# Performance work log

Measured on AMD Instinct MI355X. Metric: run time of the kernel, lower is better.

Reference implementation:

```python
import jax, jax.numpy as jnp
import numpy as np

PAD = 0  # module-level global in the original repo (MT convention)


def setup_inputs() -> dict:
    key = jax.random.key(0)
    k1, k2, k3 = jax.random.split(key, 3)
    N, V, D = 2048, 32000, 512
    # realistic log-probabilities over the vocab
    pred_ll = jax.nn.log_softmax(jax.random.normal(k1, (N, V), jnp.float32), axis=-1)
    target = jax.random.randint(k2, (N,), 0, V)
    # frozen pretrained word-vector table (nn.Embedding.from_pretrained)
    emb = jax.random.normal(k3, (V, D), jnp.float32)
    return {"pred_ll": pred_ll, "target": target, "emb": emb}


def reference(pred_ll, target, emb):
    # pred_ll: [N, V] log-probs; target: [N] int ids; emb: [V, D] frozen table
    mask = (target != PAD).astype(pred_ll.dtype)  # [N] non-pad mask

    # nll_loss = -pred_ll.gather(-1, target) summed over non-pad tokens
    nll = -jnp.take_along_axis(pred_ll, target[:, None], axis=-1)[:, 0]  # [N]
    nll_loss = jnp.sum(nll * mask)

    # pairwise L2 distance gold-embedding vs full table, via the GEMM identity
    # ||g - e||^2 = ||g||^2 + ||e||^2 - 2 g.e  (avoids the [N, V, D] tensor)
    g = emb[target]                                    # [N, D]
    g2 = jnp.sum(g * g, axis=-1, keepdims=True)        # [N, 1]
    e2 = jnp.sum(emb * emb, axis=-1)[None, :]          # [1, V]
    d2 = jnp.maximum(g2 + e2 - 2.0 * (g @ emb.T), 0.0)  # [N, V]
    dist = jnp.sqrt(jnp.maximum(d2, 1e-12))             # [N, V], L2 distances

    dist_max = jnp.max(dist, axis=1, keepdims=True)    # [N, 1]
    w = jax.nn.softmax(dist_max - jnp.abs(dist), axis=1)  # [N, V]

    # loss = sum_v softmax_weight * (-log p), summed over non-pad tokens
    loss = jnp.sum(w * (-pred_ll), axis=1)             # [N]
    return (jnp.sum(loss * mask), nll_loss)
```

## Files before the change

### kernel.cpp

```cpp
#include <hip/hip_runtime.h>
#include <hip/hip_bf16.h>
#include <float.h>

#define NTOK   2048
#define VOCAB  32000
#define DIM    512
#define NCHUNK 128
#define NTILES 2000
#define ROWSB  256
#define NRB    (NTOK / ROWSB)
#define TILE_BYTES 16384

typedef __attribute__((ext_vector_type(4))) float  f32x4;
typedef __attribute__((ext_vector_type(8))) short  bf16x8;
typedef unsigned int u32;

__device__ __forceinline__ short f2bf(float f) {
    unsigned u = __builtin_bit_cast(unsigned, f);
    u = (u + 0x7FFFu + ((u >> 16) & 1u)) >> 16;
    return (short)u;
}

__device__ __forceinline__ void async_copy16(void* lds, const void* g) {
    __builtin_amdgcn_global_load_lds(
        (const __attribute__((address_space(1))) u32*)(const u32*)g,
        (__attribute__((address_space(3))) u32*)(u32*)lds, 16, 0, 0);
}

__global__ void init_out(float* out) {
    if (threadIdx.x < 2) out[threadIdx.x] = 0.f;
}

__global__ __launch_bounds__(256) void precast_kernel(
    const float* __restrict__ emb, short* __restrict__ Bbf, float* __restrict__ e2) {
    const int tile = blockIdx.x;
    const int t = threadIdx.x, w = t >> 6, l = t & 63;
    const int v0 = tile * 16;
    char* tbase = (char*)Bbf + (size_t)tile * TILE_BYTES;
    #pragma unroll
    for (int it = 0; it < 4; ++it) {
        const int v = it * 4 + w;
        const int j = l;
        const float* src = emb + (size_t)(v0 + v) * DIM + j * 8;
        f32x4 x0 = *(const f32x4*)src;
        f32x4 x1 = *(const f32x4*)(src + 4);
        bf16x8 b;
        b[0]=f2bf(x0.x); b[1]=f2bf(x0.y); b[2]=f2bf(x0.z); b[3]=f2bf(x0.w);
        b[4]=f2bf(x1.x); b[5]=f2bf(x1.y); b[6]=f2bf(x1.z); b[7]=f2bf(x1.w);
        float sq = x0.x*x0.x + x0.y*x0.y + x0.z*x0.z + x0.w*x0.w
                 + x1.x*x1.x + x1.y*x1.y + x1.z*x1.z + x1.w*x1.w;
        #pragma unroll
        for (int m = 1; m < 64; m <<= 1) sq += __shfl_xor(sq, m);
        if (l == 0) e2[v0 + v] = sq;
        const int addr = v * 1024 + ((j * 16) ^ ((v & 7) << 4));
        *(bf16x8*)(tbase + addr) = b;
    }
}

__global__ __launch_bounds__(256) void e2_kernel(const float* __restrict__ emb,
                                                 float* __restrict__ e2) {
    int gid = blockIdx.x * 256 + threadIdx.x;
    int wid = gid >> 6, l = gid & 63;
    if (wid >= VOCAB) return;
    const float* row = emb + (size_t)wid * DIM + l * 8;
    f32x4 a = *(const f32x4*)row;
    f32x4 b = *(const f32x4*)(row + 4);
    float s = a.x*a.x + a.y*a.y + a.z*a.z + a.w*a.w
            + b.x*b.x + b.y*b.y + b.z*b.z + b.w*b.w;
    #pragma unroll
    for (int m = 1; m < 64; m <<= 1) s += __shfl_xor(s, m);
    if (l == 0) e2[wid] = s;
}

template<bool PRECAST>
__global__ __launch_bounds__(512, 2) void fused_kernel(
    const float* __restrict__ pred_ll, const int* __restrict__ target,
    const float* __restrict__ emb, const short* __restrict__ Bbf,
    const float* __restrict__ e2g,
    float* __restrict__ partials ) {

    const int rb = blockIdx.x;
    const int ch = blockIdx.y;
    const int t  = threadIdx.x;
    const int w  = t >> 6;
    const int l  = t & 63;
    const int l15 = l & 15;
    const int lg  = l >> 4;

    __shared__ short ldsb[2][16 * DIM];

    const int t0 = (ch * NTILES) >> 7;
    const int t1 = ((ch + 1) * NTILES) >> 7;
    const int rowbase = rb * ROWSB + w * 32;

    bf16x8 afrag[2][16];
    #pragma unroll
    for (int s = 0; s < 2; ++s) {
        const int grow = target[rowbase + s * 16 + l15];
        if constexpr (PRECAST) {
            const char* abase = (const char*)Bbf + (size_t)(grow >> 4) * TILE_BYTES
                              + (grow & 15) * 1024;
            const int aswz = (grow & 7) << 4;
            #pragma unroll
            for (int ks = 0; ks < 16; ++ks)
                afrag[s][ks] = *(const bf16x8*)(abase + (((ks * 4 + lg) * 16) ^ aswz));
        } else {
            const float* gsrc = emb + (size_t)grow * DIM;
            #pragma unroll
            for (int ks = 0; ks < 16; ++ks) {
                const int k0 = ks * 32 + lg * 8;
                f32x4 x0 = *(const f32x4*)(gsrc + k0);
                f32x4 x1 = *(const f32x4*)(gsrc + k0 + 4);
                bf16x8 a;
                a[0]=f2bf(x0.x); a[1]=f2bf(x0.y); a[2]=f2bf(x0.z); a[3]=f2bf(x0.w);
                a[4]=f2bf(x1.x); a[5]=f2bf(x1.y); a[6]=f2bf(x1.z); a[7]=f2bf(x1.w);
                afrag[s][ks] = a;
            }
        }
    }
    float g2[2][4];
    #pragma unroll
    for (int s = 0; s < 2; ++s)
        #pragma unroll
        for (int r = 0; r < 4; ++r)
            g2[s][r] = e2g[target[rowbase + s * 16 + lg * 4 + r]];

    float s_[2][4] = {{0,0,0,0},{0,0,0,0}};
    float ac_[2][4] = {{0,0,0,0},{0,0,0,0}};

    auto stage = [&](int buf, int tg) {
        if constexpr (PRECAST) {
            const char* src = (const char*)Bbf + (size_t)tg * TILE_BYTES;
            char* dst = (char*)&ldsb[buf][0];
            async_copy16(dst + t * 16, src + t * 16);
            async_copy16(dst + 8192 + t * 16, src + 8192 + t * 16);
        } else {
            const int v0 = tg * 16;
            #pragma unroll
            for (int it = 0; it < 2; ++it) {
                const int c = it * 512 + t;
                const int v = c >> 6, j = c & 63;
                const float* src = emb + (size_t)(v0 + v) * DIM + j * 8;
                f32x4 x0 = *(const f32x4*)src;
                f32x4 x1 = *(const f32x4*)(src + 4);
                bf16x8 b;
                b[0]=f2bf(x0.x); b[1]=f2bf(x0.y); b[2]=f2bf(x0.z); b[3]=f2bf(x0.w);
                b[4]=f2bf(x1.x); b[5]=f2bf(x1.y); b[6]=f2bf(x1.z); b[7]=f2bf(x1.w);
                const int addr = v * 1024 + ((j * 16) ^ ((v & 7) << 4));
                *(bf16x8*)((char*)&ldsb[buf][0] + addr) = b;
            }
        }
    };

    stage(0, t0);
    __syncthreads();

    int cur = 0;
    const int swz = (l15 & 7) << 4;
    for (int tg = t0; tg < t1; ++tg) {
        if (tg + 1 < t1) stage(cur ^ 1, tg + 1);

        const int v0 = tg * 16;
        const float e2v = e2g[v0 + l15];
        float q[2][4];
        {
            const size_t p0 = (size_t)rowbase * VOCAB + v0 + l15;
            #pragma unroll
            for (int s = 0; s < 2; ++s)
                #pragma unroll
                for (int r = 0; r < 4; ++r)
                    q[s][r] = pred_ll[p0 + (size_t)(s * 16 + lg * 4 + r) * VOCAB];
        }

        f32x4 accs[2] = {{0,0,0,0},{0,0,0,0}};
        const char* lb = (const char*)&ldsb[cur][0];
        #pragma unroll
        for (int ks = 0; ks < 16; ++ks) {
            const int inner = (ks * 64 + lg * 16) ^ swz;
            bf16x8 b = *(const bf16x8*)(lb + l15 * 1024 + inner);
            accs[0] = __builtin_amdgcn_mfma_f32_16x16x32_bf16(afrag[0][ks], b, accs[0], 0, 0, 0);
            accs[1] = __builtin_amdgcn_mfma_f32_16x16x32_bf16(afrag[1][ks], b, accs[1], 0, 0, 0);
        }

        #pragma unroll
        for (int s = 0; s < 2; ++s)
            #pragma unroll
            for (int r = 0; r < 4; ++r) {
                float d2 = fmaxf(fmaf(-2.f, accs[s][r], g2[s][r] + e2v), 1e-12f);
                const float e = __expf(-sqrtf(d2));
                s_[s][r] += e;
                ac_[s][r] = fmaf(e, -q[s][r], ac_[s][r]);
            }

        __syncthreads();
        cur ^= 1;
    }

    #pragma unroll
    for (int s = 0; s < 2; ++s)
        #pragma unroll
        for (int r = 0; r < 4; ++r) {
            float sv = s_[s][r], av = ac_[s][r];
            #pragma unroll
            for (int m = 1; m < 16; m <<= 1) {
                sv += __shfl_xor(sv, m);
                av += __shfl_xor(av, m);
            }
            if (l15 == 0) {
                const int rg = rowbase + s * 16 + lg * 4 + r;
                float* pp = partials + ((size_t)rg * NCHUNK + ch) * 2;
                pp[0] = sv; pp[1] = av;
            }
        }
}

__global__ __launch_bounds__(256) void reduce_kernel(
    const float* __restrict__ pred_ll, const int* __restrict__ target,
    const float* __restrict__ partials, float* __restrict__ out) {
    const int row = blockIdx.x * 256 + threadIdx.x;
    float loss = 0.f, nll = 0.f;
    if (row < NTOK) {
        const int tg = target[row];
        const float mask = (tg != 0) ? 1.f : 0.f;
        const float* pp = partials + (size_t)row * NCHUNK * 2;
        float S = 0.f, A = 0.f;
        #pragma unroll 8
        for (int c = 0; c < NCHUNK; ++c) { S += pp[c * 2]; A += pp[c * 2 + 1]; }
        loss = mask * (A / S);
        nll  = mask * (-pred_ll[(size_t)row * VOCAB + tg]);
    }
    #pragma unroll
    for (int o = 32; o > 0; o >>= 1) {
        loss += __shfl_xor(loss, o);
        nll  += __shfl_xor(nll, o);
    }
    if ((threadIdx.x & 63) == 0) {
        atomicAdd(&out[0], loss);
        atomicAdd(&out[1], nll);
    }
}

extern "C" void kernel_launch(void* const* d_in, const int* in_sizes, int n_in,
                              void* d_out, int out_size, void* d_ws, size_t ws_size,
                              hipStream_t stream) {
    const float* pred_ll = (const float*)d_in[0];
    const int*   target  = (const int*)d_in[1];
    const float* emb     = (const float*)d_in[2];
    float* out = (float*)d_out;

    float* e2       = (float*)d_ws;
    float* partials = e2 + VOCAB;
    const size_t base = (size_t)VOCAB * 4 + (size_t)NTOK * NCHUNK * 2 * 4;
    short* Bbf      = (short*)((char*)d_ws + base);
    const size_t need = base + (size_t)NTILES * TILE_BYTES;
    const bool precast = (ws_size >= need);

    hipLaunchKernelGGL(init_out, dim3(1), dim3(64), 0, stream, out);
    if (precast) {
        hipLaunchKernelGGL(precast_kernel, dim3(NTILES), dim3(256), 0, stream, emb, Bbf, e2);
        hipLaunchKernelGGL((fused_kernel<true>), dim3(NRB, NCHUNK), dim3(512), 0, stream,
                           pred_ll, target, emb, Bbf, e2, partials);
    } else {
        hipLaunchKernelGGL(e2_kernel, dim3(VOCAB * 64 / 256), dim3(256), 0, stream, emb, e2);
        hipLaunchKernelGGL((fused_kernel<false>), dim3(NRB, NCHUNK), dim3(512), 0, stream,
                           pred_ll, target, emb, Bbf, e2, partials);
    }
    hipLaunchKernelGGL(reduce_kernel, dim3(NTOK / 256), dim3(256), 0, stream,
                       pred_ll, target, partials, out);
}
```

Baseline: 180.4 us.

## Stage pred_ll tiles into LDS asynchronously and halve block rows

```diff
diff --git a/kernel.cpp b/kernel.cpp
--- a/kernel.cpp
+++ b/kernel.cpp
@@ -7,9 +7,10 @@
 #define DIM    512
 #define NCHUNK 128
 #define NTILES 2000
-#define ROWSB  256
+#define ROWSB  128
 #define NRB    (NTOK / ROWSB)
 #define TILE_BYTES 16384
+#define QTILE_BYTES 8192
 
 typedef __attribute__((ext_vector_type(4))) float  f32x4;
 typedef __attribute__((ext_vector_type(8))) short  bf16x8;
@@ -25,6 +26,10 @@
     __builtin_amdgcn_global_load_lds(
         (const __attribute__((address_space(1))) u32*)(const u32*)g,
         (__attribute__((address_space(3))) u32*)(u32*)lds, 16, 0, 0);
+}
+
+__device__ __forceinline__ int qswz(int addr) {
+    return addr ^ (((addr >> 8) & 1) << 6);
 }
 
 __global__ void init_out(float* out) {
@@ -73,7 +78,7 @@
 }
 
 template<bool PRECAST>
-__global__ __launch_bounds__(512, 2) void fused_kernel(
+__global__ __launch_bounds__(256, 2) void fused_kernel(
     const float* __restrict__ pred_ll, const int* __restrict__ target,
     const float* __restrict__ emb, const short* __restrict__ Bbf,
     const float* __restrict__ e2g,
@@ -87,11 +92,13 @@
     const int l15 = l & 15;
     const int lg  = l >> 4;
 
-    __shared__ short ldsb[2][16 * DIM];
+    __shared__ char ldsB[2][TILE_BYTES];
+    __shared__ char ldsQ[2][QTILE_BYTES];
 
     const int t0 = (ch * NTILES) >> 7;
     const int t1 = ((ch + 1) * NTILES) >> 7;
-    const int rowbase = rb * ROWSB + w * 32;
+    const int rowblk = rb * ROWSB;
+    const int rowbase = rowblk + w * 32;
 
     bf16x8 afrag[2][16];
     #pragma unroll
@@ -129,51 +136,66 @@
     float ac_[2][4] = {{0,0,0,0},{0,0,0,0}};
 
     auto stage = [&](int buf, int tg) {
+        const int v0 = tg * 16;
         if constexpr (PRECAST) {
-            const char* src = (const char*)Bbf + (size_t)tg * TILE_BYTES;
-            char* dst = (char*)&ldsb[buf][0];
-            async_copy16(dst + t * 16, src + t * 16);
-            async_copy16(dst + 8192 + t * 16, src + 8192 + t * 16);
+            const char* srcB = (const char*)Bbf + (size_t)tg * TILE_BYTES;
+            char* dstB = ldsB[buf];
+            #pragma unroll
+            for (int it = 0; it < 4; ++it)
+                async_copy16(dstB + it * 4096 + t * 16, srcB + it * 4096 + t * 16);
         } else {
-            const int v0 = tg * 16;
             #pragma unroll
             for (int it = 0; it < 2; ++it) {
-                const int c = it * 512 + t;
-                const int v = c >> 6, j = c & 63;
-                const float* src = emb + (size_t)(v0 + v) * DIM + j * 8;
+                const int c = it * 256 + t;
+                const int v = c >> 5, j = c & 31;
+                const float* src = emb + (size_t)(v0 + v) * DIM + j * 16;
                 f32x4 x0 = *(const f32x4*)src;
                 f32x4 x1 = *(const f32x4*)(src + 4);
-                bf16x8 b;
-                b[0]=f2bf(x0.x); b[1]=f2bf(x0.y); b[2]=f2bf(x0.z); b[3]=f2bf(x0.w);
-                b[4]=f2bf(x1.x); b[5]=f2bf(x1.y); b[6]=f2bf(x1.z); b[7]=f2bf(x1.w);
-                const int addr = v * 1024 + ((j * 16) ^ ((v & 7) << 4));
-                *(bf16x8*)((char*)&ldsb[buf][0] + addr) = b;
-            }
+                f32x4 x2 = *(const f32x4*)(src + 8);
+                f32x4 x3 = *(const f32x4*)(src + 12);
+                bf16x8 b0, b1;
+                b0[0]=f2bf(x0.x); b0[1]=f2bf(x0.y); b0[2]=f2bf(x0.z); b0[3]=f2bf(x0.w);
+                b0[4]=f2bf(x1.x); b0[5]=f2bf(x1.y); b0[6]=f2bf(x1.z); b0[7]=f2bf(x1.w);
+                b1[0]=f2bf(x2.x); b1[1]=f2bf(x2.y); b1[2]=f2bf(x2.z); b1[3]=f2bf(x2.w);
+                b1[4]=f2bf(x3.x); b1[5]=f2bf(x3.y); b1[6]=f2bf(x3.z); b1[7]=f2bf(x3.w);
+                const int a0 = v * 1024 + (((j * 2    ) * 16) ^ ((v & 7) << 4));
+                const int a1 = v * 1024 + (((j * 2 + 1) * 16) ^ ((v & 7) << 4));
+                *(bf16x8*)(ldsB[buf] + a0) = b0;
+                *(bf16x8*)(ldsB[buf] + a1) = b1;
+            }
+        }
+        char* dstQ = ldsQ[buf];
+        #pragma unroll
+        for (int it = 0; it < 2; ++it) {
+            const int p = (it * 256 + t) * 16;
+            const int a = qswz(p);
+            const int row = a >> 6, c16 = (a >> 4) & 3;
+            const float* src = pred_ll + (size_t)(rowblk + row) * VOCAB + v0 + c16 * 4;
+            async_copy16(dstQ + p, src);
         }
     };
 
     stage(0, t0);
-    __syncthreads();
 
     int cur = 0;
     const int swz = (l15 & 7) << 4;
     for (int tg = t0; tg < t1; ++tg) {
-        if (tg + 1 < t1) stage(cur ^ 1, tg + 1);
+        if (tg + 1 < t1) {
+            stage(cur ^ 1, tg + 1);
+            if constexpr (PRECAST)
+                asm volatile("s_waitcnt vmcnt(6)" ::: "memory");
+            else
+                asm volatile("s_waitcnt vmcnt(2) lgkmcnt(0)" ::: "memory");
+        } else {
+            asm volatile("s_waitcnt vmcnt(0) lgkmcnt(0)" ::: "memory");
+        }
+        __builtin_amdgcn_s_barrier();
 
         const int v0 = tg * 16;
         const float e2v = e2g[v0 + l15];
-        float q[2][4];
-        {
-            const size_t p0 = (size_t)rowbase * VOCAB + v0 + l15;
-            #pragma unroll
-            for (int s = 0; s < 2; ++s)
-                #pragma unroll
-                for (int r = 0; r < 4; ++r)
-                    q[s][r] = pred_ll[p0 + (size_t)(s * 16 + lg * 4 + r) * VOCAB];
-        }
 
         f32x4 accs[2] = {{0,0,0,0},{0,0,0,0}};
-        const char* lb = (const char*)&ldsb[cur][0];
+        const char* lb = ldsB[cur];
         #pragma unroll
         for (int ks = 0; ks < 16; ++ks) {
             const int inner = (ks * 64 + lg * 16) ^ swz;
@@ -182,17 +204,21 @@
             accs[1] = __builtin_amdgcn_mfma_f32_16x16x32_bf16(afrag[1][ks], b, accs[1], 0, 0, 0);
         }
 
+        const char* lq = ldsQ[cur];
         #pragma unroll
         for (int s = 0; s < 2; ++s)
             #pragma unroll
             for (int r = 0; r < 4; ++r) {
+                const int rloc = w * 32 + s * 16 + lg * 4 + r;
+                const float q = *(const float*)(lq + qswz(rloc * 64 + l15 * 4));
                 float d2 = fmaxf(fmaf(-2.f, accs[s][r], g2[s][r] + e2v), 1e-12f);
                 const float e = __expf(-sqrtf(d2));
                 s_[s][r] += e;
-                ac_[s][r] = fmaf(e, -q[s][r], ac_[s][r]);
-            }
-
-        __syncthreads();
+                ac_[s][r] = fmaf(e, -q, ac_[s][r]);
+            }
+
+        asm volatile("" ::: "memory");
+        __builtin_amdgcn_s_barrier();
         cur ^= 1;
     }
 
@@ -258,11 +284,11 @@
     hipLaunchKernelGGL(init_out, dim3(1), dim3(64), 0, stream, out);
     if (precast) {
         hipLaunchKernelGGL(precast_kernel, dim3(NTILES), dim3(256), 0, stream, emb, Bbf, e2);
-        hipLaunchKernelGGL((fused_kernel<true>), dim3(NRB, NCHUNK), dim3(512), 0, stream,
+        hipLaunchKernelGGL((fused_kernel<true>), dim3(NRB, NCHUNK), dim3(256), 0, stream,
                            pred_ll, target, emb, Bbf, e2, partials);
     } else {
         hipLaunchKernelGGL(e2_kernel, dim3(VOCAB * 64 / 256), dim3(256), 0, stream, emb, e2);
-        hipLaunchKernelGGL((fused_kernel<false>), dim3(NRB, NCHUNK), dim3(512), 0, stream,
+        hipLaunchKernelGGL((fused_kernel<false>), dim3(NRB, NCHUNK), dim3(256), 0, stream,
                            pred_ll, target, emb, Bbf, e2, partials);
     }
     hipLaunchKernelGGL(reduce_kernel, dim3(NTOK / 256), dim3(256), 0, stream,
```

New measurement: 179.6 us. Within noise of the previous version (-0.4%).

## Load B fragments directly to registers, dropping LDS staging and block sync

Applied to the files above, without the earlier changes.

```diff
diff --git a/kernel.cpp b/kernel.cpp
--- a/kernel.cpp
+++ b/kernel.cpp
@@ -7,13 +7,12 @@
 #define DIM    512
 #define NCHUNK 128
 #define NTILES 2000
-#define ROWSB  256
+#define ROWSB  128
 #define NRB    (NTOK / ROWSB)
 #define TILE_BYTES 16384
 
 typedef __attribute__((ext_vector_type(4))) float  f32x4;
 typedef __attribute__((ext_vector_type(8))) short  bf16x8;
-typedef unsigned int u32;
 
 __device__ __forceinline__ short f2bf(float f) {
     unsigned u = __builtin_bit_cast(unsigned, f);
@@ -21,10 +20,11 @@
     return (short)u;
 }
 
-__device__ __forceinline__ void async_copy16(void* lds, const void* g) {
-    __builtin_amdgcn_global_load_lds(
-        (const __attribute__((address_space(1))) u32*)(const u32*)g,
-        (__attribute__((address_space(3))) u32*)(u32*)lds, 16, 0, 0);
+__device__ __forceinline__ bf16x8 cvt8(f32x4 a, f32x4 b) {
+    bf16x8 r;
+    r[0]=f2bf(a.x); r[1]=f2bf(a.y); r[2]=f2bf(a.z); r[3]=f2bf(a.w);
+    r[4]=f2bf(b.x); r[5]=f2bf(b.y); r[6]=f2bf(b.z); r[7]=f2bf(b.w);
+    return r;
 }
 
 __global__ void init_out(float* out) {
@@ -40,20 +40,16 @@
     #pragma unroll
     for (int it = 0; it < 4; ++it) {
         const int v = it * 4 + w;
-        const int j = l;
-        const float* src = emb + (size_t)(v0 + v) * DIM + j * 8;
+        const float* src = emb + (size_t)(v0 + v) * DIM + l * 8;
         f32x4 x0 = *(const f32x4*)src;
         f32x4 x1 = *(const f32x4*)(src + 4);
-        bf16x8 b;
-        b[0]=f2bf(x0.x); b[1]=f2bf(x0.y); b[2]=f2bf(x0.z); b[3]=f2bf(x0.w);
-        b[4]=f2bf(x1.x); b[5]=f2bf(x1.y); b[6]=f2bf(x1.z); b[7]=f2bf(x1.w);
         float sq = x0.x*x0.x + x0.y*x0.y + x0.z*x0.z + x0.w*x0.w
                  + x1.x*x1.x + x1.y*x1.y + x1.z*x1.z + x1.w*x1.w;
         #pragma unroll
         for (int m = 1; m < 64; m <<= 1) sq += __shfl_xor(sq, m);
         if (l == 0) e2[v0 + v] = sq;
-        const int addr = v * 1024 + ((j * 16) ^ ((v & 7) << 4));
-        *(bf16x8*)(tbase + addr) = b;
+        char* dst = tbase + (l >> 2) * 1024 + (((l & 3) * 16 + v) * 16);
+        *(bf16x8*)dst = cvt8(x0, x1);
     }
 }
 
@@ -73,7 +69,7 @@
 }
 
 template<bool PRECAST>
-__global__ __launch_bounds__(512, 2) void fused_kernel(
+__global__ __launch_bounds__(256, 2) void fused_kernel(
     const float* __restrict__ pred_ll, const int* __restrict__ target,
     const float* __restrict__ emb, const short* __restrict__ Bbf,
     const float* __restrict__ e2g,
@@ -82,12 +78,10 @@
     const int rb = blockIdx.x;
     const int ch = blockIdx.y;
     const int t  = threadIdx.x;
-    const int w  = t >> 6;
     const int l  = t & 63;
     const int l15 = l & 15;
     const int lg  = l >> 4;
-
-    __shared__ short ldsb[2][16 * DIM];
+    const int w   = t >> 6;
 
     const int t0 = (ch * NTILES) >> 7;
     const int t1 = ((ch + 1) * NTILES) >> 7;
@@ -98,23 +92,18 @@
     for (int s = 0; s < 2; ++s) {
         const int grow = target[rowbase + s * 16 + l15];
         if constexpr (PRECAST) {
-            const char* abase = (const char*)Bbf + (size_t)(grow >> 4) * TILE_BYTES
-                              + (grow & 15) * 1024;
-            const int aswz = (grow & 7) << 4;
+            const char* ab = (const char*)Bbf + (size_t)(grow >> 4) * TILE_BYTES
+                           + ((l & 48) + (grow & 15)) * 16;
             #pragma unroll
             for (int ks = 0; ks < 16; ++ks)
-                afrag[s][ks] = *(const bf16x8*)(abase + (((ks * 4 + lg) * 16) ^ aswz));
+                afrag[s][ks] = *(const bf16x8*)(ab + ks * 1024);
         } else {
             const float* gsrc = emb + (size_t)grow * DIM;
             #pragma unroll
             for (int ks = 0; ks < 16; ++ks) {
                 const int k0 = ks * 32 + lg * 8;
-                f32x4 x0 = *(const f32x4*)(gsrc + k0);
-                f32x4 x1 = *(const f32x4*)(gsrc + k0 + 4);
-                bf16x8 a;
-                a[0]=f2bf(x0.x); a[1]=f2bf(x0.y); a[2]=f2bf(x0.z); a[3]=f2bf(x0.w);
-                a[4]=f2bf(x1.x); a[5]=f2bf(x1.y); a[6]=f2bf(x1.z); a[7]=f2bf(x1.w);
-                afrag[s][ks] = a;
+                afrag[s][ks] = cvt8(*(const f32x4*)(gsrc + k0),
+                                    *(const f32x4*)(gsrc + k0 + 4));
             }
         }
     }
@@ -128,38 +117,29 @@
     float s_[2][4] = {{0,0,0,0},{0,0,0,0}};
     float ac_[2][4] = {{0,0,0,0},{0,0,0,0}};
 
-    auto stage = [&](int buf, int tg) {
+    auto loadq = [&](int tg, int qp, bf16x8* dst) {
         if constexpr (PRECAST) {
-            const char* src = (const char*)Bbf + (size_t)tg * TILE_BYTES;
-            char* dst = (char*)&ldsb[buf][0];
-            async_copy16(dst + t * 16, src + t * 16);
-            async_copy16(dst + 8192 + t * 16, src + 8192 + t * 16);
+            const char* src = (const char*)Bbf + (size_t)tg * TILE_BYTES
+                            + qp * 4096 + l * 16;
+            #pragma unroll
+            for (int k = 0; k < 4; ++k)
+                dst[k] = *(const bf16x8*)(src + k * 1024);
         } else {
-            const int v0 = tg * 16;
-            #pragma unroll
-            for (int it = 0; it < 2; ++it) {
-                const int c = it * 512 + t;
-                const int v = c >> 6, j = c & 63;
-                const float* src = emb + (size_t)(v0 + v) * DIM + j * 8;
-                f32x4 x0 = *(const f32x4*)src;
-                f32x4 x1 = *(const f32x4*)(src + 4);
-                bf16x8 b;
-                b[0]=f2bf(x0.x); b[1]=f2bf(x0.y); b[2]=f2bf(x0.z); b[3]=f2bf(x0.w);
-                b[4]=f2bf(x1.x); b[5]=f2bf(x1.y); b[6]=f2bf(x1.z); b[7]=f2bf(x1.w);
-                const int addr = v * 1024 + ((j * 16) ^ ((v & 7) << 4));
-                *(bf16x8*)((char*)&ldsb[buf][0] + addr) = b;
+            const float* bsrc = emb + (size_t)(tg * 16 + l15) * DIM;
+            #pragma unroll
+            for (int k = 0; k < 4; ++k) {
+                const int k0 = (qp * 4 + k) * 32 + lg * 8;
+                dst[k] = cvt8(*(const f32x4*)(bsrc + k0),
+                              *(const f32x4*)(bsrc + k0 + 4));
             }
         }
     };
 
-    stage(0, t0);
-    __syncthreads();
-
-    int cur = 0;
-    const int swz = (l15 & 7) << 4;
+    bf16x8 buf[2][4];
+    loadq(t0, 0, buf[0]);
+
+    #pragma unroll 1
     for (int tg = t0; tg < t1; ++tg) {
-        if (tg + 1 < t1) stage(cur ^ 1, tg + 1);
-
         const int v0 = tg * 16;
         const float e2v = e2g[v0 + l15];
         float q[2][4];
@@ -173,13 +153,18 @@
         }
 
         f32x4 accs[2] = {{0,0,0,0},{0,0,0,0}};
-        const char* lb = (const char*)&ldsb[cur][0];
-        #pragma unroll
-        for (int ks = 0; ks < 16; ++ks) {
-            const int inner = (ks * 64 + lg * 16) ^ swz;
-            bf16x8 b = *(const bf16x8*)(lb + l15 * 1024 + inner);
-            accs[0] = __builtin_amdgcn_mfma_f32_16x16x32_bf16(afrag[0][ks], b, accs[0], 0, 0, 0);
-            accs[1] = __builtin_amdgcn_mfma_f32_16x16x32_bf16(afrag[1][ks], b, accs[1], 0, 0, 0);
+        #pragma unroll
+        for (int qp = 0; qp < 4; ++qp) {
+            const int ntg = (qp == 3) ? ((tg + 1 < t1) ? tg + 1 : tg) : tg;
+            const int nqp = (qp + 1) & 3;
+            loadq(ntg, nqp, buf[(qp + 1) & 1]);
+            #pragma unroll
+            for (int k = 0; k < 4; ++k) {
+                accs[0] = __builtin_amdgcn_mfma_f32_16x16x32_bf16(
+                    afrag[0][qp * 4 + k], buf[qp & 1][k], accs[0], 0, 0, 0);
+                accs[1] = __builtin_amdgcn_mfma_f32_16x16x32_bf16(
+                    afrag[1][qp * 4 + k], buf[qp & 1][k], accs[1], 0, 0, 0);
+            }
         }
 
         #pragma unroll
@@ -192,8 +177,7 @@
                 ac_[s][r] = fmaf(e, -q[s][r], ac_[s][r]);
             }
 
-        __syncthreads();
-        cur ^= 1;
+        if (((tg - t0) & 3) == 3) __builtin_amdgcn_s_barrier();
     }
 
     #pragma unroll
@@ -258,11 +242,11 @@
     hipLaunchKernelGGL(init_out, dim3(1), dim3(64), 0, stream, out);
     if (precast) {
         hipLaunchKernelGGL(precast_kernel, dim3(NTILES), dim3(256), 0, stream, emb, Bbf, e2);
-        hipLaunchKernelGGL((fused_kernel<true>), dim3(NRB, NCHUNK), dim3(512), 0, stream,
+        hipLaunchKernelGGL((fused_kernel<true>), dim3(NRB, NCHUNK), dim3(256), 0, stream,
                            pred_ll, target, emb, Bbf, e2, partials);
     } else {
         hipLaunchKernelGGL(e2_kernel, dim3(VOCAB * 64 / 256), dim3(256), 0, stream, emb, e2);
-        hipLaunchKernelGGL((fused_kernel<false>), dim3(NRB, NCHUNK), dim3(512), 0, stream,
+        hipLaunchKernelGGL((fused_kernel<false>), dim3(NRB, NCHUNK), dim3(256), 0, stream,
                            pred_ll, target, emb, Bbf, e2, partials);
     }
     hipLaunchKernelGGL(reduce_kernel, dim3(NTOK / 256), dim3(256), 0, stream,
```

Measured after the change: 242.8 us. 1.35x slower.
